# Kernel tuning notes

Hardware: AMD Instinct MI355X
Metric: run time of the kernel (lower is better)

Reference implementation:

```python
import jax, jax.numpy as jnp
import numpy as np

B = 4096       # batch
D = 256        # num_features
H = 512        # proposal_hidden_units
K = 10         # mixture_components
C = 64         # context_units
L = 4          # proposal_residual_blocks
S = 10         # num_importance_samples (call default)
HEAD = 3 * K + C
LOG2PI = float(np.log(2.0 * np.pi))


def setup_inputs() -> dict:
    key = jax.random.key(0)
    ks = jax.random.split(key, 10)
    x = jax.random.normal(ks[0], (B, D), jnp.float32)
    observed_mask = (jax.random.uniform(ks[1], (B, D)) < 0.5).astype(jnp.float32)
    s_in = 1.0 / np.sqrt(2 * D)
    s_h = 1.0 / np.sqrt(H)
    W_in = (jax.random.normal(ks[2], (2 * D, H), jnp.float32) * s_in)
    b_in = jnp.zeros((H,), jnp.float32)
    W1 = jax.random.normal(ks[3], (L, H, H), jnp.float32) * s_h
    b1 = jnp.zeros((L, H), jnp.float32)
    W2 = jax.random.normal(ks[4], (L, H, H), jnp.float32) * s_h
    b2 = jnp.zeros((L, H), jnp.float32)
    W_fin = jax.random.normal(ks[5], (H, D * HEAD), jnp.float32) * s_h
    b_fin = jnp.zeros((D * HEAD,), jnp.float32)
    return {
        "x": x, "observed_mask": observed_mask,
        "W_in": W_in, "b_in": b_in,
        "W1": W1, "b1": b1, "W2": W2, "b2": b2,
        "W_fin": W_fin, "b_fin": b_fin,
        "num_importance_samples": S,
    }


def _proposal_params(x_o, observed_mask, W_in, b_in, W1, b1, W2, b2, W_fin, b_fin):
    # Residual MLP proposal network on [x_o, observed_mask].
    h = jnp.concatenate([x_o, observed_mask], axis=-1) @ W_in + b_in  # [B, H]
    for l in range(L):
        r = jax.nn.relu(h) @ W1[l] + b1[l]
        r = jax.nn.relu(r) @ W2[l] + b2[l]
        h = h + r
    out = (h @ W_fin + b_fin).reshape(h.shape[0], D, HEAD)  # [B, D, 3K+C]
    logits = out[..., :K]
    means = out[..., K:2 * K]
    scales = jax.nn.softplus(out[..., 2 * K:3 * K]) + 1e-3
    return logits, means, scales


def reference(x, observed_mask, W_in, b_in, W1, b1, W2, b2, W_fin, b_fin,
              num_importance_samples):
    query = 1.0 - observed_mask
    x_o = x * observed_mask
    x_u = x * query

    logits, means, scales = _proposal_params(
        x_o, observed_mask, W_in, b_in, W1, b1, W2, b2, W_fin, b_fin)

    # Per-feature mixture-of-Gaussians log-likelihood of x_u, masked by query.
    log_w = jax.nn.log_softmax(logits, axis=-1)               # [B, D, K]
    z = (x_u[..., None] - means) / scales
    comp_ll = -0.5 * z * z - jnp.log(scales) - 0.5 * LOG2PI   # [B, D, K]
    proposal_ll = jax.scipy.special.logsumexp(log_w + comp_ll, axis=-1) * query

    # Samples (stop_gradient in the original).
    skey = jax.random.key(1234)
    kc, kn = jax.random.split(skey)
    comp = jax.random.categorical(kc, logits, axis=-1,
                                  shape=(num_importance_samples,) + logits.shape[:2])  # [S, B, D]
    mu = jnp.take_along_axis(means[None], comp[..., None], axis=-1)[..., 0]    # [S, B, D]
    sg = jnp.take_along_axis(scales[None], comp[..., None], axis=-1)[..., 0]   # [S, B, D]
    eps = jax.random.normal(kn, comp.shape, jnp.float32)
    samples = mu + sg * eps                                   # [S, B, D]
    samples = jnp.transpose(samples, (1, 0, 2))               # [B, S, D]
    samples = jax.lax.stop_gradient(samples) * query[:, None, :]
    # call() multiplies by query twice (before and after selected_features block)
    proposal_samples = samples * query[:, None, :]

    proposal_mean = jnp.sum(jax.nn.softmax(logits, axis=-1) * means, axis=-1) * query
    proposal_mean = proposal_mean * query  # second masking, as in call()

    return proposal_ll, proposal_samples, proposal_mean
```

## Files before the change

### kernel.cpp

```cpp
#include <hip/hip_runtime.h>
#include <cstdint>

#define B 4096
#define D 256
#define H 512
#define K 10
#define NL 4
#define S 10
#define NOUT 30
#define HEADW 94
#define ND (B*D)
#define NFIN 7680
#define NLOG 2560
#define NMS  5120

typedef __bf16 bf16x8 __attribute__((ext_vector_type(8)));
typedef float  f32x16 __attribute__((ext_vector_type(16)));

__host__ __device__ inline void threefry2x32(uint32_t k0, uint32_t k1,
                                             uint32_t x0, uint32_t x1,
                                             uint32_t& o0, uint32_t& o1) {
  uint32_t ks2 = k0 ^ k1 ^ 0x1BD11BDAu;
#define TF_ROT(x, r) (((x) << (r)) | ((x) >> (32 - (r))))
#define TF_RND(r) { x0 += x1; x1 = TF_ROT(x1, r); x1 ^= x0; }
  x0 += k0; x1 += k1;
  TF_RND(13) TF_RND(15) TF_RND(26) TF_RND(6)
  x0 += k1; x1 += ks2 + 1u;
  TF_RND(17) TF_RND(29) TF_RND(16) TF_RND(24)
  x0 += ks2; x1 += k0 + 2u;
  TF_RND(13) TF_RND(15) TF_RND(26) TF_RND(6)
  x0 += k0; x1 += k1 + 3u;
  TF_RND(17) TF_RND(29) TF_RND(16) TF_RND(24)
  x0 += k1; x1 += ks2 + 4u;
  TF_RND(13) TF_RND(15) TF_RND(26) TF_RND(6)
  x0 += ks2; x1 += k0 + 5u;
  o0 = x0; o1 = x1;
#undef TF_RND
#undef TF_ROT
}

__device__ __forceinline__ uint32_t rb32(uint32_t k0, uint32_t k1, uint32_t idx) {
  uint32_t a, b;
  threefry2x32(k0, k1, 0u, idx, a, b);
  return a ^ b;
}

__device__ __forceinline__ float u01_from_bits(uint32_t bits) {
  return __uint_as_float((bits >> 9) | 0x3f800000u) - 1.0f;
}

__device__ __forceinline__ float erfinv_f32(float x) {
  float w = -log1pf(-x * x);
  float p;
  if (w < 5.0f) {
    w = w - 2.5f;
    p = 2.81022636e-08f;
    p = fmaf(p, w, 3.43273939e-07f);
    p = fmaf(p, w, -3.5233877e-06f);
    p = fmaf(p, w, -4.39150654e-06f);
    p = fmaf(p, w, 0.00021858087f);
    p = fmaf(p, w, -0.00125372503f);
    p = fmaf(p, w, -0.00417768164f);
    p = fmaf(p, w, 0.246640727f);
    p = fmaf(p, w, 1.50140941f);
  } else {
    w = sqrtf(w) - 3.0f;
    p = -0.000200214257f;
    p = fmaf(p, w, 0.000100950558f);
    p = fmaf(p, w, 0.00134934322f);
    p = fmaf(p, w, -0.00367342844f);
    p = fmaf(p, w, 0.00573950773f);
    p = fmaf(p, w, -0.0076224613f);
    p = fmaf(p, w, 0.00943887047f);
    p = fmaf(p, w, 1.00167406f);
    p = fmaf(p, w, 2.83297682f);
  }
  return p * x;
}

__device__ __forceinline__ unsigned short bf16_rne(float x) {
  uint32_t u = __float_as_uint(x);
  uint32_t r = u + 0x7fffu + ((u >> 16) & 1u);
  return (unsigned short)(r >> 16);
}

__device__ __forceinline__ void split2(float x, short& hi, short& lo) {
  unsigned short hb = bf16_rne(x);
  float hf = __uint_as_float((uint32_t)hb << 16);
  hi = (short)hb;
  lo = (short)bf16_rne(x - hf);
}

__device__ __forceinline__ void gload16(const void* g, void* l) {
  __builtin_amdgcn_global_load_lds(
      (const __attribute__((address_space(1))) void*)g,
      (__attribute__((address_space(3))) void*)l, 16, 0, 0);
}

template <int ROWS>
__device__ __forceinline__ void stage_region(const short* __restrict__ g,
                                             short* l, int wid, int lane) {
#pragma unroll
  for (int c = wid; c < ROWS / 16; c += 4) {
    const short* gp = g + (size_t)(c * 16 + (lane >> 2)) * 512 + (lane & 3) * 8;
    gload16(gp, l + c * 512);
  }
}

__global__ __launch_bounds__(256) void prep_kernel(const float* __restrict__ x,
                                                   const float* __restrict__ mask,
                                                   float* __restrict__ xcat) {
  int i = blockIdx.x * 256 + threadIdx.x;
  if (i >= B * 2 * D) return;
  int b = i >> 9, c = i & 511;
  float v = (c < D) ? x[b * D + c] * mask[b * D + c] : mask[b * D + (c - D)];
  xcat[i] = v;
}

__global__ __launch_bounds__(256) void wgatherL(const float* __restrict__ Wf,
                                                float* __restrict__ wsgL) {
  int c = blockIdx.x * 256 + threadIdx.x;
  int k = blockIdx.y;
  int dd = c / K, j = c - dd * K;
  wsgL[(size_t)k * NLOG + c] = Wf[(size_t)k * (D * HEADW) + dd * HEADW + j];
}

__global__ __launch_bounds__(256) void wsplit_ms(const float* __restrict__ Wf,
                                                 short* __restrict__ whi,
                                                 short* __restrict__ wlo) {
  __shared__ float tile[32][33];
  int n0 = blockIdx.x * 32, k0 = blockIdx.y * 32;
  int tx = threadIdx.x & 31, ty = threadIdx.x >> 5;
#pragma unroll
  for (int r = 0; r < 4; ++r) {
    int k = k0 + ty + r * 8;
    int n = n0 + tx;
    int dd = n / 20, j = n - dd * 20;
    tile[ty + r * 8][tx] = Wf[(size_t)k * (D * HEADW) + dd * HEADW + 10 + j];
  }
  __syncthreads();
#pragma unroll
  for (int r = 0; r < 4; ++r) {
    int n = n0 + ty + r * 8;
    int k = k0 + tx;
    float v = tile[tx][ty + r * 8];
    short hb, lb;
    split2(v, hb, lb);
    whi[(size_t)n * 512 + k] = hb;
    wlo[(size_t)n * 512 + k] = lb;
  }
}

template <int RELU, int RES>
__global__ __launch_bounds__(256) void gemm_trunk(const float* __restrict__ A,
                                                  const float* __restrict__ W,
                                                  const float* __restrict__ bias,
                                                  const float* res, float* C) {
  __shared__ float As[32 * 136];
  __shared__ float Ws[32 * 64];
  const int tid = threadIdx.x;
  const int lane = tid & 63, wid = tid >> 6;
  const int tx = tid & 15, ty = tid >> 4;
  const int bm = blockIdx.y * 128, bn = blockIdx.x * 64;
  const int ls = tid & 7, lm = tid >> 3;

  float acc[8][4] = {};

  for (int k0 = 0; k0 < H; k0 += 32) {
#pragma unroll
    for (int c = wid; c < 8; c += 4) {
      gload16(W + (size_t)(k0 + c * 4 + (lane >> 4)) * H + bn + (lane & 15) * 4,
              Ws + c * 256 + lane * 4);
    }
#pragma unroll
    for (int r = 0; r < 4; ++r) {
      int m = lm + 32 * r;
      float4 f = *(const float4*)(A + (size_t)(bm + m) * H + k0 + 4 * ls);
      if (RELU) {
        f.x = fmaxf(f.x, 0.0f); f.y = fmaxf(f.y, 0.0f);
        f.z = fmaxf(f.z, 0.0f); f.w = fmaxf(f.w, 0.0f);
      }
      As[(4 * ls + 0) * 136 + m] = f.x;
      As[(4 * ls + 1) * 136 + m] = f.y;
      As[(4 * ls + 2) * 136 + m] = f.z;
      As[(4 * ls + 3) * 136 + m] = f.w;
    }
    __syncthreads();
#pragma unroll
    for (int kk = 0; kk < 32; ++kk) {
      float a[8], b[4];
      *(float4*)(a + 0) = *(const float4*)(As + kk * 136 + ty * 8);
      *(float4*)(a + 4) = *(const float4*)(As + kk * 136 + ty * 8 + 4);
      *(float4*)(b + 0) = *(const float4*)(Ws + kk * 64 + tx * 4);
#pragma unroll
      for (int i = 0; i < 8; ++i)
#pragma unroll
        for (int j = 0; j < 4; ++j) acc[i][j] = fmaf(a[i], b[j], acc[i][j]);
    }
    __syncthreads();
  }
#pragma unroll
  for (int i = 0; i < 8; ++i) {
    int row = bm + ty * 8 + i;
#pragma unroll
    for (int j = 0; j < 4; ++j) {
      int col = bn + tx * 4 + j;
      float v = acc[i][j] + bias[col];
      if (RES) v = res[(size_t)row * H + col] + v;
      C[(size_t)row * H + col] = v;
    }
  }
}

__global__ __launch_bounds__(256) void gemm_logits(const float* __restrict__ A,
                                                   const float* __restrict__ Wg,
                                                   const float* __restrict__ bf,
                                                   float* __restrict__ headout) {
  __shared__ float As[32 * 136];
  __shared__ float Ws[32 * 128];
  const int tid = threadIdx.x;
  const int lane = tid & 63, wid = tid >> 6;
  const int tx = tid & 15, ty = tid >> 4;
  const int bm = blockIdx.y * 128, bn = blockIdx.x * 128;
  const int ls = tid & 7, lm = tid >> 3;

  float acc[8][8] = {};

  for (int k0 = 0; k0 < H; k0 += 32) {
#pragma unroll
    for (int c = wid; c < 16; c += 4) {
      gload16(Wg + (size_t)(k0 + c * 2 + (lane >> 5)) * NLOG + bn + (lane & 31) * 4,
              Ws + c * 256 + lane * 4);
    }
#pragma unroll
    for (int r = 0; r < 4; ++r) {
      int m = lm + 32 * r;
      float4 f = *(const float4*)(A + (size_t)(bm + m) * H + k0 + 4 * ls);
      As[(4 * ls + 0) * 136 + m] = f.x;
      As[(4 * ls + 1) * 136 + m] = f.y;
      As[(4 * ls + 2) * 136 + m] = f.z;
      As[(4 * ls + 3) * 136 + m] = f.w;
    }
    __syncthreads();
#pragma unroll
    for (int kk = 0; kk < 32; ++kk) {
      float a[8], b[8];
      *(float4*)(a + 0) = *(const float4*)(As + kk * 136 + ty * 8);
      *(float4*)(a + 4) = *(const float4*)(As + kk * 136 + ty * 8 + 4);
      *(float4*)(b + 0) = *(const float4*)(Ws + kk * 128 + tx * 8);
      *(float4*)(b + 4) = *(const float4*)(Ws + kk * 128 + tx * 8 + 4);
#pragma unroll
      for (int i = 0; i < 8; ++i)
#pragma unroll
        for (int j = 0; j < 8; ++j) acc[i][j] = fmaf(a[i], b[j], acc[i][j]);
    }
    __syncthreads();
  }
#pragma unroll
  for (int i = 0; i < 8; ++i) {
    int row = bm + ty * 8 + i;
#pragma unroll
    for (int j = 0; j < 8; ++j) {
      int c = bn + tx * 8 + j;
      int dd = c / K, jj = c - dd * K;
      float v = acc[i][j] + bf[dd * HEADW + jj];
      headout[(size_t)row * NFIN + dd * NOUT + jj] = v;
    }
  }
}

__global__ __launch_bounds__(256) void gemm_ms(const float* __restrict__ A,
                                               const short* __restrict__ Bh,
                                               const short* __restrict__ Bl,
                                               const float* __restrict__ bf,
                                               float* __restrict__ headout) {
  __shared__ short lds[4 * 128 * 32];
  const int tid = threadIdx.x;
  const int lane = tid & 63, wid = tid >> 6;
  const int wm = wid >> 1, wn = wid & 1;
  const int bm = blockIdx.y * 128, bn = blockIdx.x * 128;
  const int ls = tid & 7, lm = tid >> 3;

  short* ldsAh = lds;
  short* ldsAl = lds + 4096;
  short* ldsBh = lds + 8192;
  short* ldsBl = lds + 12288;

  const short* gBh = Bh + (size_t)bn * 512;
  const short* gBl = Bl + (size_t)bn * 512;

  f32x16 acc[2][2];
#pragma unroll
  for (int mt = 0; mt < 2; ++mt)
#pragma unroll
    for (int nt = 0; nt < 2; ++nt)
#pragma unroll
      for (int i = 0; i < 16; ++i) acc[mt][nt][i] = 0.0f;

  for (int k0 = 0; k0 < 512; k0 += 32) {
    stage_region<128>(gBh + k0, ldsBh, wid, lane);
    stage_region<128>(gBl + k0, ldsBl, wid, lane);
#pragma unroll
    for (int r = 0; r < 4; ++r) {
      int m = lm + 32 * r;
      float4 f = *(const float4*)(A + (size_t)(bm + m) * H + k0 + 4 * ls);
      short4 h4, l4;
      split2(f.x, h4.x, l4.x); split2(f.y, h4.y, l4.y);
      split2(f.z, h4.z, l4.z); split2(f.w, h4.w, l4.w);
      *(short4*)(ldsAh + m * 32 + 4 * ls) = h4;
      *(short4*)(ldsAl + m * 32 + 4 * ls) = l4;
    }
    __syncthreads();
#pragma unroll
    for (int sub = 0; sub < 2; ++sub) {
      bf16x8 ah[2], al[2], bh[2], bl[2];
#pragma unroll
      for (int mt = 0; mt < 2; ++mt) {
        int r = wm * 64 + mt * 32 + (lane & 31);
        int off = r * 32 + sub * 16 + (lane >> 5) * 8;
        ah[mt] = *(const bf16x8*)(ldsAh + off);
        al[mt] = *(const bf16x8*)(ldsAl + off);
      }
#pragma unroll
      for (int nt = 0; nt < 2; ++nt) {
        int r = wn * 64 + nt * 32 + (lane & 31);
        int off = r * 32 + sub * 16 + (lane >> 5) * 8;
        bh[nt] = *(const bf16x8*)(ldsBh + off);
        bl[nt] = *(const bf16x8*)(ldsBl + off);
      }
#pragma unroll
      for (int mt = 0; mt < 2; ++mt)
#pragma unroll
        for (int nt = 0; nt < 2; ++nt) {
          acc[mt][nt] = __builtin_amdgcn_mfma_f32_32x32x16_bf16(ah[mt], bh[nt], acc[mt][nt], 0, 0, 0);
          acc[mt][nt] = __builtin_amdgcn_mfma_f32_32x32x16_bf16(ah[mt], bl[nt], acc[mt][nt], 0, 0, 0);
          acc[mt][nt] = __builtin_amdgcn_mfma_f32_32x32x16_bf16(al[mt], bh[nt], acc[mt][nt], 0, 0, 0);
        }
    }
    __syncthreads();
  }

#pragma unroll
  for (int mt = 0; mt < 2; ++mt)
#pragma unroll
    for (int nt = 0; nt < 2; ++nt) {
      int col = bn + wn * 64 + nt * 32 + (lane & 31);
      int rbase = bm + wm * 64 + mt * 32 + 4 * (lane >> 5);
      int dd = col / 20, j = col - dd * 20;
#pragma unroll
      for (int reg = 0; reg < 16; ++reg) {
        int row = rbase + (reg & 3) + 8 * (reg >> 2);
        float v = acc[mt][nt][reg] + bf[dd * HEADW + 10 + j];
        if (j >= 10) v = (fmaxf(v, 0.0f) + log1pf(expf(-fabsf(v)))) + 0.001f;
        headout[(size_t)row * NFIN + dd * NOUT + 10 + j] = v;
      }
    }
}

__global__ __launch_bounds__(256) void fused_tail(const float* __restrict__ head,
                                                  const float* __restrict__ x,
                                                  const float* __restrict__ mask,
                                                  float* __restrict__ out_ll,
                                                  float* __restrict__ out_s,
                                                  float* __restrict__ out_mean,
                                                  uint32_t kc0, uint32_t kc1,
                                                  uint32_t kn0, uint32_t kn1) {
  int idx = blockIdx.x * 256 + threadIdx.x;
  if (idx >= ND) return;
  int b = idx >> 8, d = idx & (D - 1);
  const float* hp = head + (size_t)idx * NOUT;
  float lg[K], mn[K], sc[K];
#pragma unroll
  for (int k = 0; k < K; ++k) { lg[k] = hp[k]; mn[k] = hp[K + k]; sc[k] = hp[2 * K + k]; }
  float q = 1.0f - mask[idx];
  float xu = x[idx] * q;
  float m = lg[0];
#pragma unroll
  for (int k = 1; k < K; ++k) m = fmaxf(m, lg[k]);
  float e[K];
  float sum = 0.0f;
#pragma unroll
  for (int k = 0; k < K; ++k) { e[k] = expf(lg[k] - m); sum += e[k]; }
  float lse = logf(sum);
  float a[K];
  float amax = -3.402823466e38f;
#pragma unroll
  for (int k = 0; k < K; ++k) {
    float z = (xu - mn[k]) / sc[k];
    float cll = -0.5f * z * z - logf(sc[k]) - 0.9189385332046727f;
    float lw = (lg[k] - m) - lse;
    a[k] = lw + cll;
    amax = fmaxf(amax, a[k]);
  }
  float s2 = 0.0f;
#pragma unroll
  for (int k = 0; k < K; ++k) s2 += expf(a[k] - amax);
  out_ll[idx] = (logf(s2) + amax) * q;
  float pm = 0.0f;
#pragma unroll
  for (int k = 0; k < K; ++k) pm += (e[k] / sum) * mn[k];
  out_mean[idx] = pm * q;
  for (int s = 0; s < S; ++s) {
    uint32_t t32 = (uint32_t)s * (uint32_t)ND + (uint32_t)idx;
    uint32_t base = t32 * (uint32_t)K;
    int best = 0;
    float vbest = -3.402823466e38f;
#pragma unroll
    for (int k = 0; k < K; ++k) {
      uint32_t bits = rb32(kc0, kc1, base + (uint32_t)k);
      float f = fmaxf(u01_from_bits(bits), 1.17549435e-38f);
      float g = -logf(-logf(f));
      float v = g + lg[k];
      if (v > vbest) { vbest = v; best = k; }
    }
    uint32_t ebits = rb32(kn0, kn1, t32);
    float f = u01_from_bits(ebits);
    float r = f * 2.0f + (-0.99999994f);
    r = fmaxf(r, -0.99999994f);
    float eps = 1.4142135623730951f * erfinv_f32(r);
    out_s[((size_t)b * S + s) * D + d] = (mn[best] + sc[best] * eps) * q;
  }
}

extern "C" void kernel_launch(void* const* d_in, const int* in_sizes, int n_in,
                              void* d_out, int out_size, void* d_ws, size_t ws_size,
                              hipStream_t stream) {
  const float* x    = (const float*)d_in[0];
  const float* mask = (const float*)d_in[1];
  const float* W_in = (const float*)d_in[2];
  const float* b_in = (const float*)d_in[3];
  const float* W1   = (const float*)d_in[4];
  const float* b1   = (const float*)d_in[5];
  const float* W2   = (const float*)d_in[6];
  const float* b2   = (const float*)d_in[7];
  const float* Wf   = (const float*)d_in[8];
  const float* bf   = (const float*)d_in[9];

  char* w = (char*)d_ws;
  float* head  = (float*)w;
  float* xcat  = head;
  float* t     = head;
  float* h     = (float*)(w + 125829120);
  float* wsgL  = (float*)(w + 134217728);
  short* wms_h = (short*)(w + 139460608);
  short* wms_l = (short*)(w + 144703488);

  float* out_ll   = (float*)d_out;
  float* out_s    = out_ll + (size_t)ND;
  float* out_mean = out_s + (size_t)ND * S;

  wgatherL<<<dim3(NLOG / 256, 512), 256, 0, stream>>>(Wf, wsgL);
  wsplit_ms<<<dim3(NMS / 32, 512 / 32), 256, 0, stream>>>(Wf, wms_h, wms_l);

  prep_kernel<<<(B * 2 * D) / 256, 256, 0, stream>>>(x, mask, xcat);

  dim3 gtr(H / 64, B / 128);
  gemm_trunk<0, 0><<<gtr, 256, 0, stream>>>(xcat, W_in, b_in, nullptr, h);
  for (int l = 0; l < NL; ++l) {
    gemm_trunk<1, 0><<<gtr, 256, 0, stream>>>(h, W1 + (size_t)l * H * H,
                                              b1 + (size_t)l * H, nullptr, t);
    gemm_trunk<1, 1><<<gtr, 256, 0, stream>>>(t, W2 + (size_t)l * H * H,
                                              b2 + (size_t)l * H, h, h);
  }

  gemm_logits<<<dim3(NLOG / 128, B / 128), 256, 0, stream>>>(h, wsgL, bf, head);
  gemm_ms<<<dim3(NMS / 128, B / 128), 256, 0, stream>>>(h, wms_h, wms_l, bf, head);

  uint32_t kc0, kc1, kn0, kn1;
  threefry2x32(0u, 1234u, 0u, 0u, kc0, kc1);
  threefry2x32(0u, 1234u, 0u, 1u, kn0, kn1);
  fused_tail<<<ND / 256, 256, 0, stream>>>(head, x, mask, out_ll, out_s, out_mean,
                                           kc0, kc1, kn0, kn1);
}
```

Baseline: 1.322 ms.

## Skip tail work for observed entries, shrink trunk GEMM tiles, simplify Gumbel sampling

Adds a compaction pass that zeroes the outputs for observed positions and builds a list of unobserved indices via an atomic counter, so the expensive sampling tail runs only on query entries. The Gumbel-max categorical draw is replaced by an exponential-race form (argmin of -log2(u)/exp(logit)), which drops one log per draw and uses a fast log2. Trunk GEMMs switch to 64x64 tiles with 128 threads, doubling the block count. The exponential race breaks ties differently near u=0, the global atomic serializes list building, and the compacted list scatters memory access in the tail.

```diff
diff --git a/kernel.cpp b/kernel.cpp
--- a/kernel.cpp
+++ b/kernel.cpp
@@ -152,45 +152,45 @@
 }
 
 template <int RELU, int RES>
-__global__ __launch_bounds__(256) void gemm_trunk(const float* __restrict__ A,
+__global__ __launch_bounds__(128) void gemm_trunk(const float* __restrict__ A,
                                                   const float* __restrict__ W,
                                                   const float* __restrict__ bias,
                                                   const float* res, float* C) {
-  __shared__ float As[32 * 136];
+  __shared__ float As[32 * 68];
   __shared__ float Ws[32 * 64];
   const int tid = threadIdx.x;
   const int lane = tid & 63, wid = tid >> 6;
   const int tx = tid & 15, ty = tid >> 4;
-  const int bm = blockIdx.y * 128, bn = blockIdx.x * 64;
+  const int bm = blockIdx.y * 64, bn = blockIdx.x * 64;
   const int ls = tid & 7, lm = tid >> 3;
 
   float acc[8][4] = {};
 
   for (int k0 = 0; k0 < H; k0 += 32) {
 #pragma unroll
-    for (int c = wid; c < 8; c += 4) {
+    for (int c = wid; c < 8; c += 2) {
       gload16(W + (size_t)(k0 + c * 4 + (lane >> 4)) * H + bn + (lane & 15) * 4,
               Ws + c * 256 + lane * 4);
     }
 #pragma unroll
     for (int r = 0; r < 4; ++r) {
-      int m = lm + 32 * r;
+      int m = lm + 16 * r;
       float4 f = *(const float4*)(A + (size_t)(bm + m) * H + k0 + 4 * ls);
       if (RELU) {
         f.x = fmaxf(f.x, 0.0f); f.y = fmaxf(f.y, 0.0f);
         f.z = fmaxf(f.z, 0.0f); f.w = fmaxf(f.w, 0.0f);
       }
-      As[(4 * ls + 0) * 136 + m] = f.x;
-      As[(4 * ls + 1) * 136 + m] = f.y;
-      As[(4 * ls + 2) * 136 + m] = f.z;
-      As[(4 * ls + 3) * 136 + m] = f.w;
+      As[(4 * ls + 0) * 68 + m] = f.x;
+      As[(4 * ls + 1) * 68 + m] = f.y;
+      As[(4 * ls + 2) * 68 + m] = f.z;
+      As[(4 * ls + 3) * 68 + m] = f.w;
     }
     __syncthreads();
 #pragma unroll
     for (int kk = 0; kk < 32; ++kk) {
       float a[8], b[4];
-      *(float4*)(a + 0) = *(const float4*)(As + kk * 136 + ty * 8);
-      *(float4*)(a + 4) = *(const float4*)(As + kk * 136 + ty * 8 + 4);
+      *(float4*)(a + 0) = *(const float4*)(As + kk * 68 + ty * 8);
+      *(float4*)(a + 4) = *(const float4*)(As + kk * 68 + ty * 8 + 4);
       *(float4*)(b + 0) = *(const float4*)(Ws + kk * 64 + tx * 4);
 #pragma unroll
       for (int i = 0; i < 8; ++i)
@@ -357,16 +357,43 @@
     }
 }
 
+__global__ __launch_bounds__(256) void init_counter(int* counter) {
+  if (threadIdx.x == 0 && blockIdx.x == 0) *counter = 0;
+}
+
+__global__ __launch_bounds__(256) void compact_zero(const float* __restrict__ mask,
+                                                    float* __restrict__ out_ll,
+                                                    float* __restrict__ out_s,
+                                                    float* __restrict__ out_mean,
+                                                    int* __restrict__ list,
+                                                    int* __restrict__ counter) {
+  int idx = blockIdx.x * 256 + threadIdx.x;
+  if (idx >= ND) return;
+  if (mask[idx] != 0.0f) {
+    int b = idx >> 8, d = idx & (D - 1);
+    out_ll[idx] = 0.0f;
+    out_mean[idx] = 0.0f;
+#pragma unroll
+    for (int s = 0; s < S; ++s) out_s[((size_t)b * S + s) * D + d] = 0.0f;
+  } else {
+    int pos = atomicAdd(counter, 1);
+    list[pos] = idx;
+  }
+}
+
 __global__ __launch_bounds__(256) void fused_tail(const float* __restrict__ head,
                                                   const float* __restrict__ x,
                                                   const float* __restrict__ mask,
+                                                  const int* __restrict__ list,
+                                                  const int* __restrict__ counter,
                                                   float* __restrict__ out_ll,
                                                   float* __restrict__ out_s,
                                                   float* __restrict__ out_mean,
                                                   uint32_t kc0, uint32_t kc1,
                                                   uint32_t kn0, uint32_t kn1) {
-  int idx = blockIdx.x * 256 + threadIdx.x;
-  if (idx >= ND) return;
+  int i = blockIdx.x * 256 + threadIdx.x;
+  if (i >= *counter) return;
+  int idx = list[i];
   int b = idx >> 8, d = idx & (D - 1);
   const float* hp = head + (size_t)idx * NOUT;
   float lg[K], mn[K], sc[K];
@@ -400,24 +427,27 @@
 #pragma unroll
   for (int k = 0; k < K; ++k) pm += (e[k] / sum) * mn[k];
   out_mean[idx] = pm * q;
+  float inv_e[K];
+#pragma unroll
+  for (int k = 0; k < K; ++k) inv_e[k] = 1.0f / e[k];
   for (int s = 0; s < S; ++s) {
     uint32_t t32 = (uint32_t)s * (uint32_t)ND + (uint32_t)idx;
     uint32_t base = t32 * (uint32_t)K;
     int best = 0;
-    float vbest = -3.402823466e38f;
+    float rbest = 3.402823466e38f;
 #pragma unroll
     for (int k = 0; k < K; ++k) {
       uint32_t bits = rb32(kc0, kc1, base + (uint32_t)k);
-      float f = fmaxf(u01_from_bits(bits), 1.17549435e-38f);
-      float g = -logf(-logf(f));
-      float v = g + lg[k];
-      if (v > vbest) { vbest = v; best = k; }
+      float u = u01_from_bits(bits);
+      float wv = -__log2f(u);
+      float r = wv * inv_e[k];
+      if (r < rbest) { rbest = r; best = k; }
     }
     uint32_t ebits = rb32(kn0, kn1, t32);
     float f = u01_from_bits(ebits);
-    float r = f * 2.0f + (-0.99999994f);
-    r = fmaxf(r, -0.99999994f);
-    float eps = 1.4142135623730951f * erfinv_f32(r);
+    float r2 = f * 2.0f + (-0.99999994f);
+    r2 = fmaxf(r2, -0.99999994f);
+    float eps = 1.4142135623730951f * erfinv_f32(r2);
     out_s[((size_t)b * S + s) * D + d] = (mn[best] + sc[best] * eps) * q;
   }
 }
@@ -437,13 +467,15 @@
   const float* bf   = (const float*)d_in[9];
 
   char* w = (char*)d_ws;
-  float* head  = (float*)w;
-  float* xcat  = head;
-  float* t     = head;
-  float* h     = (float*)(w + 125829120);
-  float* wsgL  = (float*)(w + 134217728);
-  short* wms_h = (short*)(w + 139460608);
-  short* wms_l = (short*)(w + 144703488);
+  float* head   = (float*)w;
+  float* xcat   = head;
+  float* t      = head;
+  float* h      = (float*)(w + 125829120);
+  float* wsgL   = (float*)(w + 134217728);
+  int*   list   = (int*)(w + 134217728);
+  short* wms_h  = (short*)(w + 139460608);
+  short* wms_l  = (short*)(w + 144703488);
+  int*   counter = (int*)(w + 149946368);
 
   float* out_ll   = (float*)d_out;
   float* out_s    = out_ll + (size_t)ND;
@@ -454,21 +486,26 @@
 
   prep_kernel<<<(B * 2 * D) / 256, 256, 0, stream>>>(x, mask, xcat);
 
-  dim3 gtr(H / 64, B / 128);
-  gemm_trunk<0, 0><<<gtr, 256, 0, stream>>>(xcat, W_in, b_in, nullptr, h);
+  dim3 gtr(H / 64, B / 64);
+  gemm_trunk<0, 0><<<gtr, 128, 0, stream>>>(xcat, W_in, b_in, nullptr, h);
   for (int l = 0; l < NL; ++l) {
-    gemm_trunk<1, 0><<<gtr, 256, 0, stream>>>(h, W1 + (size_t)l * H * H,
+    gemm_trunk<1, 0><<<gtr, 128, 0, stream>>>(h, W1 + (size_t)l * H * H,
                                               b1 + (size_t)l * H, nullptr, t);
-    gemm_trunk<1, 1><<<gtr, 256, 0, stream>>>(t, W2 + (size_t)l * H * H,
+    gemm_trunk<1, 1><<<gtr, 128, 0, stream>>>(t, W2 + (size_t)l * H * H,
                                               b2 + (size_t)l * H, h, h);
   }
 
   gemm_logits<<<dim3(NLOG / 128, B / 128), 256, 0, stream>>>(h, wsgL, bf, head);
   gemm_ms<<<dim3(NMS / 128, B / 128), 256, 0, stream>>>(h, wms_h, wms_l, bf, head);
+
+  init_counter<<<1, 256, 0, stream>>>(counter);
+  compact_zero<<<ND / 256, 256, 0, stream>>>(mask, out_ll, out_s, out_mean,
+                                             list, counter);
 
   uint32_t kc0, kc1, kn0, kn1;
   threefry2x32(0u, 1234u, 0u, 0u, kc0, kc1);
   threefry2x32(0u, 1234u, 0u, 1u, kn0, kn1);
-  fused_tail<<<ND / 256, 256, 0, stream>>>(head, x, mask, out_ll, out_s, out_mean,
+  fused_tail<<<ND / 256, 256, 0, stream>>>(head, x, mask, list, counter,
+                                           out_ll, out_s, out_mean,
                                            kc0, kc1, kn0, kn1);
 }
```

Measured after the change: 1.369 ms. 1.04x slower.
